# Optimization experiments

Hardware: AMD Instinct MI355X
Metric: run time of the kernel (lower is better)

Reference implementation:

```python
import jax, jax.numpy as jnp
import numpy as np

N_HEADS = 16
D_MODEL = 1024
D_K = D_MODEL // N_HEADS


def setup_inputs() -> dict:
    key = jax.random.key(0)
    ks = jax.random.split(key, 7)
    B, S = 2, 2048
    init = 0.02
    return {
        "query": jax.random.normal(ks[0], (B, S, D_MODEL), dtype=jnp.float32),
        "key": jax.random.normal(ks[1], (B, S, D_MODEL), dtype=jnp.float32),
        "value": jax.random.normal(ks[2], (B, S, D_MODEL), dtype=jnp.float32),
        "W_q": jax.random.normal(ks[3], (D_MODEL, D_MODEL), dtype=jnp.float32) * init,
        "W_k": jax.random.normal(ks[4], (D_MODEL, D_MODEL), dtype=jnp.float32) * init,
        "W_v": jax.random.normal(ks[5], (D_MODEL, D_MODEL), dtype=jnp.float32) * init,
        "W_o": jax.random.normal(ks[6], (D_MODEL, D_MODEL), dtype=jnp.float32) * init,
    }


def _split_heads(x):
    # (B, S, d_model) -> (B, H, S, d_k)
    B, S, _ = x.shape
    return x.reshape(B, S, N_HEADS, D_K).transpose(0, 2, 1, 3)


def reference(query, key, value, W_q, W_k, W_v, W_o):
    scale = jnp.sqrt(jnp.asarray(D_K, dtype=query.dtype))
    # torch Linear: y = x @ W.T
    Q = _split_heads(query @ W_q.T)   # (B,H,Sq,dk)
    K = _split_heads(key @ W_k.T)     # (B,H,Sk,dk)
    V = _split_heads(value @ W_v.T)   # (B,H,Sk,dk)
    scores = jnp.einsum("bhqd,bhkd->bhqk", Q, K) / scale
    attn = jax.nn.softmax(scores, axis=-1)           # (B,H,Sq,Sk); dropout p=0 -> identity
    attn_weights = attn.mean(axis=1)                 # (B,Sq,Sk) interpretable weights
    head_out = jnp.einsum("bhqk,bhkd->bqhd", attn, V)  # (B,Sq,H,dk)
    # NOTE: the original computes a head-gating (W_h) whose result is overwritten
    # by the concat below -> dead code, omitted.
    B, Sq = head_out.shape[0], head_out.shape[1]
    out = head_out.reshape(B, Sq, D_MODEL) @ W_o.T   # (B,Sq,d_model)
    return (out, attn_weights)
```

## Files before the change

kernel.cpp:

```cpp
#include <hip/hip_runtime.h>
#include <hip/hip_bf16.h>

#define Bq 2
#define Hh 16
#define Ss 2048
#define Dm 1024
#define Dk 64
#define QSC 0.18033688f

typedef _Float16 f16x8 __attribute__((ext_vector_type(8)));
typedef _Float16 f16x4 __attribute__((ext_vector_type(4)));
typedef _Float16 f16x2 __attribute__((ext_vector_type(2)));
typedef float    f32x4 __attribute__((ext_vector_type(4)));


__device__ __forceinline__ void gl_lds16(const void* g, void* lds) {
    __builtin_amdgcn_global_load_lds(
        (const __attribute__((address_space(1))) void*)g,
        (__attribute__((address_space(3))) void*)lds, 16, 0, 0);
}

extern "C" __device__ float __ocml_exp2_f32(float);

__device__ __forceinline__ float exp2_fast(float x) {
#if __has_builtin(__builtin_amdgcn_exp2f)
    return __builtin_amdgcn_exp2f(x);
#else
    return __ocml_exp2_f32(x);
#endif
}

__device__ __forceinline__ float rcp_fast(float x) {
#if __has_builtin(__builtin_amdgcn_rcpf)
    return __builtin_amdgcn_rcpf(x);
#else
    float r; asm("v_rcp_f32 %0, %1" : "=v"(r) : "v"(x)); return r;
#endif
}

__device__ __forceinline__ f16x2 pk_f16(float a, float b) {
    return __builtin_bit_cast(f16x2, __builtin_amdgcn_cvt_pkrtz(a, b));
}

__global__ __launch_bounds__(256) void convert_kernel(
    const float* __restrict__ q, const float* __restrict__ k,
    const float* __restrict__ v, const float* __restrict__ wq,
    const float* __restrict__ wk, const float* __restrict__ wv,
    const float* __restrict__ wo,
    _Float16* __restrict__ qd, _Float16* __restrict__ kd,
    _Float16* __restrict__ vd, _Float16* __restrict__ wd)
{
    int seg = blockIdx.y;
    const float* src; _Float16* dst; int n4;
    switch (seg) {
        case 0: src = q; dst = qd; n4 = 1048576; break;
        case 1: src = k; dst = kd; n4 = 1048576; break;
        case 2: src = v; dst = vd; n4 = 1048576; break;
        default:
            src = (seg == 3) ? wq : (seg == 4) ? wk : (seg == 5) ? wv : wo;
            dst = wd + (size_t)(seg - 3) * 1048576;
            n4 = 262144;
    }
    for (int i = blockIdx.x * 256 + threadIdx.x; i < n4; i += gridDim.x * 256) {
        float4 x = ((const float4*)src)[i];
        f16x4 h = {(_Float16)x.x, (_Float16)x.y, (_Float16)x.z, (_Float16)x.w};
        ((f16x4*)dst)[i] = h;
    }
}

__global__ __launch_bounds__(256) void gemm_qkv(
    const _Float16* __restrict__ qf, const _Float16* __restrict__ kf,
    const _Float16* __restrict__ vf, const _Float16* __restrict__ Wh,
    _Float16* __restrict__ Qd, _Float16* __restrict__ Kd,
    _Float16* __restrict__ Vd)
{
    __shared__ _Float16 As[128 * 32];
    __shared__ _Float16 Ws[128 * 32];
    int z = blockIdx.z;
    const _Float16* A = (z == 0) ? qf : (z == 1) ? kf : vf;
    const _Float16* W = Wh + (size_t)z * (Dm * Dm);
    int t = threadIdx.x, lane = t & 63, w = t >> 6;
    int quad = lane >> 4, l15 = lane & 15;
    int wm = w & 1, wn = w >> 1;
    int n0 = blockIdx.x * 128, m0 = blockIdx.y * 128;

    f32x4 acc[4][4] = {};
    for (int k0 = 0; k0 < Dm; k0 += 32) {
        __syncthreads();
        for (int j = 0; j < 2; ++j) {
            int ca = w * 128 + j * 64 + lane;
            int row = ca >> 2, c8 = (ca & 3) * 8;
            gl_lds16(&A[(size_t)(m0 + row) * Dm + k0 + c8],
                     &As[(size_t)(w * 128 + j * 64) * 8]);
            gl_lds16(&W[(size_t)(n0 + row) * Dm + k0 + c8],
                     &Ws[(size_t)(w * 128 + j * 64) * 8]);
        }
        __syncthreads();
        f16x8 af[4], bf[4];
        for (int mi = 0; mi < 4; ++mi)
            af[mi] = *(const f16x8*)&As[(wm * 64 + mi * 16 + l15) * 32 + quad * 8];
        for (int ni = 0; ni < 4; ++ni)
            bf[ni] = *(const f16x8*)&Ws[(wn * 64 + ni * 16 + l15) * 32 + quad * 8];
        for (int mi = 0; mi < 4; ++mi)
            for (int ni = 0; ni < 4; ++ni)
                acc[mi][ni] = __builtin_amdgcn_mfma_f32_16x16x32_f16(
                    af[mi], bf[ni], acc[mi][ni], 0, 0, 0);
    }
    _Float16* Y = (z == 0) ? Qd : (z == 1) ? Kd : Vd;
    float osc = (z == 0) ? QSC : 1.0f;
    for (int mi = 0; mi < 4; ++mi)
        for (int ni = 0; ni < 4; ++ni)
            for (int r = 0; r < 4; ++r) {
                int m = m0 + wm * 64 + mi * 16 + quad * 4 + r;
                int n = n0 + wn * 64 + ni * 16 + l15;
                int b = m >> 11, s = m & (Ss - 1);
                int h = n >> 6,  d = n & 63;
                _Float16 v = (_Float16)(acc[mi][ni][r] * osc);
                if (z < 2)
                    Y[(((size_t)(b * Hh + h) * Ss + s) << 6) + d] = v;
                else
                    Y[((size_t)(b * Hh + h) * Dk + d) * Ss + s] = v;
            }
}

__global__ __launch_bounds__(256) void gemm_out(
    const _Float16* __restrict__ HO, const _Float16* __restrict__ Woh,
    float* __restrict__ out)
{
    __shared__ _Float16 As[128 * 32];
    __shared__ _Float16 Ws[64 * 32];
    int t = threadIdx.x, lane = t & 63, w = t >> 6;
    int quad = lane >> 4, l15 = lane & 15;
    int n0 = blockIdx.x * 64, m0 = blockIdx.y * 128;

    f32x4 acc[2][4] = {};
    for (int k0 = 0; k0 < Dm; k0 += 32) {
        __syncthreads();
        for (int j = 0; j < 2; ++j) {
            int ca = w * 128 + j * 64 + lane;
            int row = ca >> 2, c8 = (ca & 3) * 8;
            gl_lds16(&HO[(size_t)(m0 + row) * Dm + k0 + c8],
                     &As[(size_t)(w * 128 + j * 64) * 8]);
        }
        {
            int cw = w * 64 + lane;
            int row = cw >> 2, c8 = (cw & 3) * 8;
            gl_lds16(&Woh[(size_t)(n0 + row) * Dm + k0 + c8],
                     &Ws[(size_t)(w * 64) * 8]);
        }
        __syncthreads();
        f16x8 af[2], bf[4];
        for (int mi = 0; mi < 2; ++mi)
            af[mi] = *(const f16x8*)&As[(w * 32 + mi * 16 + l15) * 32 + quad * 8];
        for (int ni = 0; ni < 4; ++ni)
            bf[ni] = *(const f16x8*)&Ws[(ni * 16 + l15) * 32 + quad * 8];
        for (int mi = 0; mi < 2; ++mi)
            for (int ni = 0; ni < 4; ++ni)
                acc[mi][ni] = __builtin_amdgcn_mfma_f32_16x16x32_f16(
                    af[mi], bf[ni], acc[mi][ni], 0, 0, 0);
    }
    for (int mi = 0; mi < 2; ++mi)
        for (int ni = 0; ni < 4; ++ni)
            for (int r = 0; r < 4; ++r) {
                int m = m0 + w * 32 + mi * 16 + quad * 4 + r;
                int n = n0 + ni * 16 + l15;
                out[(size_t)m * Dm + n] = acc[mi][ni][r];
            }
}

__global__ __launch_bounds__(256) void flash_kernel(
    const _Float16* __restrict__ Qh, const _Float16* __restrict__ Kh,
    const _Float16* __restrict__ Vt, _Float16* __restrict__ Op,
    float* __restrict__ lp)
{
    __shared__ alignas(16) _Float16 Ks[64][72];
    __shared__ alignas(16) _Float16 Vs[64][72];
    __shared__ alignas(16) _Float16 Ps[4][32][72];
    int t = threadIdx.x;
    int lane = t & 63, w = t >> 6;
    int quad = lane >> 4, l15 = lane & 15;
    int bh = blockIdx.x;
    int q0 = blockIdx.y * 128 + w * 32;
    int ks = blockIdx.z;
    int kt0 = ks * 16, kt1 = kt0 + 16;

    const _Float16* Qp = Qh + (size_t)bh * Ss * Dk;
    const _Float16* Kp = Kh + (size_t)bh * Ss * Dk;
    const _Float16* Vp = Vt + (size_t)bh * Dk * Ss;

    f16x8 qf[2][2];
    for (int qh = 0; qh < 2; ++qh)
        for (int kf = 0; kf < 2; ++kf)
            qf[qh][kf] = *(const f16x8*)
                &Qp[(size_t)(q0 + qh * 16 + l15) * Dk + kf * 32 + quad * 8];

    const _Float16 one = (_Float16)1.0f;
    const f16x8 ones = {one, one, one, one, one, one, one, one};

    int row0 = t >> 3,         col0 = (t & 7) * 8;
    int row1 = (256 + t) >> 3, col1 = col0;

    f16x8 kr0 = *(const f16x8*)&Kp[(size_t)(kt0 * 64 + row0) * Dk + col0];
    f16x8 kr1 = *(const f16x8*)&Kp[(size_t)(kt0 * 64 + row1) * Dk + col1];
    f16x8 vr0 = *(const f16x8*)&Vp[(size_t)row0 * Ss + kt0 * 64 + col0];
    f16x8 vr1 = *(const f16x8*)&Vp[(size_t)row1 * Ss + kt0 * 64 + col1];

    f32x4 o_acc[2][4] = {};
    f32x4 l_acc[2] = {};

    for (int kt = kt0; kt < kt1; ++kt) {
        __syncthreads();
        *(f16x8*)&Ks[row0][col0] = kr0;
        *(f16x8*)&Ks[row1][col1] = kr1;
        *(f16x8*)&Vs[row0][col0] = vr0;
        *(f16x8*)&Vs[row1][col1] = vr1;
        if (kt + 1 < kt1) {
            kr0 = *(const f16x8*)&Kp[(size_t)((kt + 1) * 64 + row0) * Dk + col0];
            kr1 = *(const f16x8*)&Kp[(size_t)((kt + 1) * 64 + row1) * Dk + col1];
            vr0 = *(const f16x8*)&Vp[(size_t)row0 * Ss + (kt + 1) * 64 + col0];
            vr1 = *(const f16x8*)&Vp[(size_t)row1 * Ss + (kt + 1) * 64 + col1];
        }
        __syncthreads();

        for (int nt = 0; nt < 4; ++nt) {
            f16x8 kf0 = *(const f16x8*)&Ks[nt * 16 + l15][quad * 8];
            f16x8 kf1 = *(const f16x8*)&Ks[nt * 16 + l15][32 + quad * 8];
            for (int qh = 0; qh < 2; ++qh) {
                f32x4 z = {};
                z = __builtin_amdgcn_mfma_f32_16x16x32_f16(kf0, qf[qh][0], z, 0, 0, 0);
                z = __builtin_amdgcn_mfma_f32_16x16x32_f16(kf1, qf[qh][1], z, 0, 0, 0);
                f16x2 h0 = pk_f16(exp2_fast(z[0]), exp2_fast(z[1]));
                f16x2 h1 = pk_f16(exp2_fast(z[2]), exp2_fast(z[3]));
                f16x4 hv = {h0[0], h0[1], h1[0], h1[1]};
                *(f16x4*)&Ps[w][qh * 16 + l15][nt * 16 + quad * 4] = hv;
            }
        }

        f16x8 vf[4][2];
        for (int dt = 0; dt < 4; ++dt) {
            vf[dt][0] = *(const f16x8*)&Vs[dt * 16 + l15][quad * 8];
            vf[dt][1] = *(const f16x8*)&Vs[dt * 16 + l15][32 + quad * 8];
        }
        for (int qh = 0; qh < 2; ++qh) {
            f16x8 pf0 = *(const f16x8*)&Ps[w][qh * 16 + l15][quad * 8];
            f16x8 pf1 = *(const f16x8*)&Ps[w][qh * 16 + l15][32 + quad * 8];
            l_acc[qh] = __builtin_amdgcn_mfma_f32_16x16x32_f16(
                pf0, ones, l_acc[qh], 0, 0, 0);
            l_acc[qh] = __builtin_amdgcn_mfma_f32_16x16x32_f16(
                pf1, ones, l_acc[qh], 0, 0, 0);
            for (int dt = 0; dt < 4; ++dt) {
                o_acc[qh][dt] = __builtin_amdgcn_mfma_f32_16x16x32_f16(
                    pf0, vf[dt][0], o_acc[qh][dt], 0, 0, 0);
                o_acc[qh][dt] = __builtin_amdgcn_mfma_f32_16x16x32_f16(
                    pf1, vf[dt][1], o_acc[qh][dt], 0, 0, 0);
            }
        }
    }

    _Float16* Od = Op + (size_t)ks * (Bq * Hh * Ss * Dk) + (size_t)bh * Ss * Dk;
    for (int qh = 0; qh < 2; ++qh) {
        for (int dt = 0; dt < 4; ++dt)
            for (int r = 0; r < 4; ++r) {
                int q = q0 + qh * 16 + quad * 4 + r;
                Od[(size_t)q * Dk + dt * 16 + l15] = (_Float16)o_acc[qh][dt][r];
            }
        if (l15 == 0)
            for (int r = 0; r < 4; ++r)
                lp[(size_t)ks * 65536 + (size_t)bh * Ss + q0 + qh * 16 +
                   quad * 4 + r] = l_acc[qh][r];
    }
}

__global__ __launch_bounds__(256) void reduce_kernel(
    const _Float16* __restrict__ Op, const float* __restrict__ lp,
    _Float16* __restrict__ HO, float* __restrict__ lw)
{
    int i = blockIdx.x * 256 + threadIdx.x;
    int d4  = i & 15;
    int row = i >> 4;
    f16x4 a = ((const f16x4*)Op)[i];
    f16x4 b = ((const f16x4*)Op)[i + 1048576];
    float l = lp[row] + lp[65536 + row];
    float inv = rcp_fast(l);
    int bh = row >> 11, q = row & (Ss - 1);
    int b_ = bh >> 4,  h = bh & 15;
    f16x4 o;
    for (int j = 0; j < 4; ++j)
        o[j] = (_Float16)(((float)a[j] + (float)b[j]) * inv);
    *(f16x4*)&HO[((size_t)(b_ * Ss + q)) * Dm + h * Dk + d4 * 4] = o;
    if (d4 == 0) lw[row] = l;
}

__global__ __launch_bounds__(256) void attn_mean_kernel(
    const _Float16* __restrict__ Qh, const _Float16* __restrict__ Kh,
    const float* __restrict__ lw, float* __restrict__ out_attn)
{
    __shared__ alignas(16) _Float16 Ks[64][72];
    int t = threadIdx.x;
    int lane = t & 63, w = t >> 6;
    int quad = lane >> 4, l15 = lane & 15;
    int k0 = blockIdx.x * 64;
    int q0 = blockIdx.y * 128;
    int b  = blockIdx.z;
    int qrow = q0 + w * 32;

    int srow0 = t >> 3, scol0 = (t & 7) * 8;
    int srow1 = (256 + t) >> 3, scol1 = scol0;

    f16x8 kr0, kr1, qn[2][2];
    float4 ln[2];
    {
        size_t base = (size_t)(b * Hh) * Ss;
        kr0 = *(const f16x8*)&Kh[(base + k0 + srow0) * Dk + scol0];
        kr1 = *(const f16x8*)&Kh[(base + k0 + srow1) * Dk + scol1];
        for (int qh = 0; qh < 2; ++qh) {
            qn[qh][0] = *(const f16x8*)&Qh[(base + qrow + qh * 16 + l15) * Dk + quad * 8];
            qn[qh][1] = *(const f16x8*)&Qh[(base + qrow + qh * 16 + l15) * Dk + 32 + quad * 8];
            ln[qh] = *(const float4*)&lw[base + qrow + qh * 16 + quad * 4];
        }
    }

    f32x4 acc[2][4] = {};
    for (int h = 0; h < Hh; ++h) {
        __syncthreads();
        *(f16x8*)&Ks[srow0][scol0] = kr0;
        *(f16x8*)&Ks[srow1][scol1] = kr1;
        f16x8 qf[2][2];
        float4 lv[2];
        for (int qh = 0; qh < 2; ++qh) {
            qf[qh][0] = qn[qh][0]; qf[qh][1] = qn[qh][1]; lv[qh] = ln[qh];
        }
        if (h < Hh - 1) {
            size_t base = (size_t)(b * Hh + h + 1) * Ss;
            kr0 = *(const f16x8*)&Kh[(base + k0 + srow0) * Dk + scol0];
            kr1 = *(const f16x8*)&Kh[(base + k0 + srow1) * Dk + scol1];
            for (int qh = 0; qh < 2; ++qh) {
                qn[qh][0] = *(const f16x8*)&Qh[(base + qrow + qh * 16 + l15) * Dk + quad * 8];
                qn[qh][1] = *(const f16x8*)&Qh[(base + qrow + qh * 16 + l15) * Dk + 32 + quad * 8];
                ln[qh] = *(const float4*)&lw[base + qrow + qh * 16 + quad * 4];
            }
        }
        __syncthreads();

        float ir[2][4];
        for (int qh = 0; qh < 2; ++qh) {
            ir[qh][0] = rcp_fast(lv[qh].x); ir[qh][1] = rcp_fast(lv[qh].y);
            ir[qh][2] = rcp_fast(lv[qh].z); ir[qh][3] = rcp_fast(lv[qh].w);
        }
        for (int nt = 0; nt < 4; ++nt) {
            f16x8 b0 = *(const f16x8*)&Ks[nt * 16 + l15][quad * 8];
            f16x8 b1 = *(const f16x8*)&Ks[nt * 16 + l15][32 + quad * 8];
            for (int qh = 0; qh < 2; ++qh) {
                f32x4 z = {};
                z = __builtin_amdgcn_mfma_f32_16x16x32_f16(qf[qh][0], b0, z, 0, 0, 0);
                z = __builtin_amdgcn_mfma_f32_16x16x32_f16(qf[qh][1], b1, z, 0, 0, 0);
                for (int r = 0; r < 4; ++r)
                    acc[qh][nt][r] += exp2_fast(z[r]) * ir[qh][r];
            }
        }
    }

    for (int qh = 0; qh < 2; ++qh)
        for (int nt = 0; nt < 4; ++nt)
            for (int r = 0; r < 4; ++r) {
                int q = qrow + qh * 16 + quad * 4 + r;
                out_attn[((size_t)(b * Ss + q)) * Ss + k0 + nt * 16 + l15] =
                    acc[qh][nt][r] * (1.0f / Hh);
            }
}

extern "C" void kernel_launch(void* const* d_in, const int* in_sizes, int n_in,
                              void* d_out, int out_size, void* d_ws, size_t ws_size,
                              hipStream_t stream) {
    const float* query = (const float*)d_in[0];
    const float* key   = (const float*)d_in[1];
    const float* value = (const float*)d_in[2];
    const float* Wq    = (const float*)d_in[3];
    const float* Wk    = (const float*)d_in[4];
    const float* Wv    = (const float*)d_in[5];
    const float* Wo    = (const float*)d_in[6];

    float* out      = (float*)d_out;
    float* attn_out = out + (size_t)4194304;

    _Float16* HO  = (_Float16*)attn_out;
    _Float16* qf  = (_Float16*)(attn_out + 2097152);
    _Float16* kf  = qf + 4194304;
    _Float16* vf  = kf + 4194304;
    _Float16* Op  = qf;
    float*    lp  = (float*)(Op + 2 * 4194304);

    _Float16* Qh = (_Float16*)d_ws;
    _Float16* Kh = Qh + (size_t)4194304;
    _Float16* Vt = Kh + (size_t)4194304;
    _Float16* Wh = Vt + (size_t)4194304;
    float*    lw = (float*)(Wh + (size_t)4194304);

    convert_kernel<<<dim3(256, 7), 256, 0, stream>>>(
        query, key, value, Wq, Wk, Wv, Wo, qf, kf, vf, Wh);

    gemm_qkv<<<dim3(8, 32, 3), 256, 0, stream>>>(qf, kf, vf, Wh, Qh, Kh, Vt);

    flash_kernel<<<dim3(Bq * Hh, Ss / 128, 2), 256, 0, stream>>>(Qh, Kh, Vt, Op, lp);

    reduce_kernel<<<4096, 256, 0, stream>>>(Op, lp, HO, lw);

    gemm_out<<<dim3(16, 32), 256, 0, stream>>>(HO, Wh + (size_t)3 * 1048576, out);

    attn_mean_kernel<<<dim3(Ss / 64, Ss / 128, Bq), 256, 0, stream>>>(
        Qh, Kh, lw, attn_out);
}
```

Measured before the change: 273.9 us.

## Double-buffer K/V via async LDS loads, keep P in registers

The flash and head-averaged attention kernels now stage K and V tiles with global_load_lds into double-buffered, XOR-swizzled LDS, so the next tile's load overlaps compute and one barrier per iteration is removed. In the flash kernel the softmax probabilities no longer go through an LDS buffer: they are rearranged into MFMA operand layout with cross-lane shuffles. The row sum is now built from scalar adds plus a final xor-shuffle reduction, replacing the extra MFMA against a ones vector. The trade-offs are many more shuffle instructions and reliance on the barrier waiting for the async loads to finish.

```diff
diff --git a/kernel.cpp b/kernel.cpp
--- a/kernel.cpp
+++ b/kernel.cpp
@@ -12,6 +12,7 @@
 typedef _Float16 f16x4 __attribute__((ext_vector_type(4)));
 typedef _Float16 f16x2 __attribute__((ext_vector_type(2)));
 typedef float    f32x4 __attribute__((ext_vector_type(4)));
+typedef unsigned int u32x4 __attribute__((ext_vector_type(4)));
 
 
 __device__ __forceinline__ void gl_lds16(const void* g, void* lds) {
@@ -38,8 +39,8 @@
 #endif
 }
 
-__device__ __forceinline__ f16x2 pk_f16(float a, float b) {
-    return __builtin_bit_cast(f16x2, __builtin_amdgcn_cvt_pkrtz(a, b));
+__device__ __forceinline__ unsigned int pk_u32(float a, float b) {
+    return __builtin_bit_cast(unsigned int, __builtin_amdgcn_cvt_pkrtz(a, b));
 }
 
 __global__ __launch_bounds__(256) void convert_kernel(
@@ -173,9 +174,7 @@
     const _Float16* __restrict__ Vt, _Float16* __restrict__ Op,
     float* __restrict__ lp)
 {
-    __shared__ alignas(16) _Float16 Ks[64][72];
-    __shared__ alignas(16) _Float16 Vs[64][72];
-    __shared__ alignas(16) _Float16 Ps[4][32][72];
+    __shared__ alignas(16) _Float16 KV[2][2][4096];
     int t = threadIdx.x;
     int lane = t & 63, w = t >> 6;
     int quad = lane >> 4, l15 = lane & 15;
@@ -185,89 +184,139 @@
     int kt0 = ks * 16, kt1 = kt0 + 16;
 
     const _Float16* Qp = Qh + (size_t)bh * Ss * Dk;
-    const _Float16* Kp = Kh + (size_t)bh * Ss * Dk;
-    const _Float16* Vp = Vt + (size_t)bh * Dk * Ss;
+    const char* Kp = (const char*)(Kh + (size_t)bh * Ss * Dk);
+    const char* Vp = (const char*)(Vt + (size_t)bh * Dk * Ss);
 
     f16x8 qf[2][2];
+#pragma unroll
     for (int qh = 0; qh < 2; ++qh)
+#pragma unroll
         for (int kf = 0; kf < 2; ++kf)
             qf[qh][kf] = *(const f16x8*)
                 &Qp[(size_t)(q0 + qh * 16 + l15) * Dk + kf * 32 + quad * 8];
 
-    const _Float16 one = (_Float16)1.0f;
-    const f16x8 ones = {one, one, one, one, one, one, one, one};
-
-    int row0 = t >> 3,         col0 = (t & 7) * 8;
-    int row1 = (256 + t) >> 3, col1 = col0;
-
-    f16x8 kr0 = *(const f16x8*)&Kp[(size_t)(kt0 * 64 + row0) * Dk + col0];
-    f16x8 kr1 = *(const f16x8*)&Kp[(size_t)(kt0 * 64 + row1) * Dk + col1];
-    f16x8 vr0 = *(const f16x8*)&Vp[(size_t)row0 * Ss + kt0 * 64 + col0];
-    f16x8 vr1 = *(const f16x8*)&Vp[(size_t)row1 * Ss + kt0 * 64 + col1];
+    int srow = t >> 3;
+    int scolb = (t & 7) * 16;
+    int iA = (((2 * quad) & 3) << 4) | l15;
+    int iB = ((((2 * quad) + 1) & 3) << 4) | l15;
+    bool lo = (quad < 2);
+    int swz = (l15 & 7) << 4;
+
+#define FSTAGE(kt, buf)                                                        \
+    {                                                                          \
+        const char* Kt = Kp + (size_t)(kt) * 8192;                             \
+        const char* Vb = Vp + (kt) * 128;                                      \
+        char* KD = (char*)&KV[buf][0][0];                                      \
+        char* VD = (char*)&KV[buf][1][0];                                      \
+        _Pragma("unroll")                                                      \
+        for (int hf = 0; hf < 2; ++hf) {                                       \
+            int r = srow + hf * 32;                                            \
+            int sc = scolb ^ ((r & 7) << 4);                                   \
+            gl_lds16(Kt + r * 128 + sc, KD + r * 128 + scolb);                 \
+            gl_lds16(Vb + (size_t)r * 4096 + sc, VD + r * 128 + scolb);        \
+        }                                                                      \
+    }
 
     f32x4 o_acc[2][4] = {};
-    f32x4 l_acc[2] = {};
-
+    float lsum[2] = {0.f, 0.f};
+
+    FSTAGE(kt0, 0);
     for (int kt = kt0; kt < kt1; ++kt) {
-        __syncthreads();
-        *(f16x8*)&Ks[row0][col0] = kr0;
-        *(f16x8*)&Ks[row1][col1] = kr1;
-        *(f16x8*)&Vs[row0][col0] = vr0;
-        *(f16x8*)&Vs[row1][col1] = vr1;
-        if (kt + 1 < kt1) {
-            kr0 = *(const f16x8*)&Kp[(size_t)((kt + 1) * 64 + row0) * Dk + col0];
-            kr1 = *(const f16x8*)&Kp[(size_t)((kt + 1) * 64 + row1) * Dk + col1];
-            vr0 = *(const f16x8*)&Vp[(size_t)row0 * Ss + (kt + 1) * 64 + col0];
-            vr1 = *(const f16x8*)&Vp[(size_t)row1 * Ss + (kt + 1) * 64 + col1];
-        }
-        __syncthreads();
-
+        int buf = (kt - kt0) & 1;
+        __syncthreads();
+        if (kt + 1 < kt1) FSTAGE(kt + 1, buf ^ 1);
+        const char* Ksb = (const char*)&KV[buf][0][0];
+        const char* Vsb = (const char*)&KV[buf][1][0];
+
+        unsigned int cu[2][4][2];
+#pragma unroll
         for (int nt = 0; nt < 4; ++nt) {
-            f16x8 kf0 = *(const f16x8*)&Ks[nt * 16 + l15][quad * 8];
-            f16x8 kf1 = *(const f16x8*)&Ks[nt * 16 + l15][32 + quad * 8];
+            int rb = (nt * 16 + l15) << 7;
+            f16x8 kf0 = *(const f16x8*)(Ksb + rb + ((quad * 16) ^ swz));
+            f16x8 kf1 = *(const f16x8*)(Ksb + rb + ((64 + quad * 16) ^ swz));
+#pragma unroll
             for (int qh = 0; qh < 2; ++qh) {
                 f32x4 z = {};
                 z = __builtin_amdgcn_mfma_f32_16x16x32_f16(kf0, qf[qh][0], z, 0, 0, 0);
                 z = __builtin_amdgcn_mfma_f32_16x16x32_f16(kf1, qf[qh][1], z, 0, 0, 0);
-                f16x2 h0 = pk_f16(exp2_fast(z[0]), exp2_fast(z[1]));
-                f16x2 h1 = pk_f16(exp2_fast(z[2]), exp2_fast(z[3]));
-                f16x4 hv = {h0[0], h0[1], h1[0], h1[1]};
-                *(f16x4*)&Ps[w][qh * 16 + l15][nt * 16 + quad * 4] = hv;
-            }
-        }
-
-        f16x8 vf[4][2];
+                float e0 = exp2_fast(z[0]), e1 = exp2_fast(z[1]);
+                float e2 = exp2_fast(z[2]), e3 = exp2_fast(z[3]);
+                lsum[qh] += (e0 + e1) + (e2 + e3);
+                cu[qh][nt][0] = pk_u32(e0, e1);
+                cu[qh][nt][1] = pk_u32(e2, e3);
+            }
+        }
+
+        f16x8 pf[2][2];
+#pragma unroll
+        for (int qh = 0; qh < 2; ++qh) {
+            unsigned int d0, d1, d2, d3, d4, d5, d6, d7;
+            {
+                unsigned int xa, xb;
+                xa = (unsigned)__shfl((int)cu[qh][0][0], iA);
+                xb = (unsigned)__shfl((int)cu[qh][1][0], iA);
+                d0 = lo ? xa : xb;
+                xa = (unsigned)__shfl((int)cu[qh][0][1], iA);
+                xb = (unsigned)__shfl((int)cu[qh][1][1], iA);
+                d1 = lo ? xa : xb;
+                xa = (unsigned)__shfl((int)cu[qh][0][0], iB);
+                xb = (unsigned)__shfl((int)cu[qh][1][0], iB);
+                d2 = lo ? xa : xb;
+                xa = (unsigned)__shfl((int)cu[qh][0][1], iB);
+                xb = (unsigned)__shfl((int)cu[qh][1][1], iB);
+                d3 = lo ? xa : xb;
+                xa = (unsigned)__shfl((int)cu[qh][2][0], iA);
+                xb = (unsigned)__shfl((int)cu[qh][3][0], iA);
+                d4 = lo ? xa : xb;
+                xa = (unsigned)__shfl((int)cu[qh][2][1], iA);
+                xb = (unsigned)__shfl((int)cu[qh][3][1], iA);
+                d5 = lo ? xa : xb;
+                xa = (unsigned)__shfl((int)cu[qh][2][0], iB);
+                xb = (unsigned)__shfl((int)cu[qh][3][0], iB);
+                d6 = lo ? xa : xb;
+                xa = (unsigned)__shfl((int)cu[qh][2][1], iB);
+                xb = (unsigned)__shfl((int)cu[qh][3][1], iB);
+                d7 = lo ? xa : xb;
+            }
+            u32x4 p0 = {d0, d1, d2, d3};
+            u32x4 p1 = {d4, d5, d6, d7};
+            pf[qh][0] = __builtin_bit_cast(f16x8, p0);
+            pf[qh][1] = __builtin_bit_cast(f16x8, p1);
+        }
+#pragma unroll
         for (int dt = 0; dt < 4; ++dt) {
-            vf[dt][0] = *(const f16x8*)&Vs[dt * 16 + l15][quad * 8];
-            vf[dt][1] = *(const f16x8*)&Vs[dt * 16 + l15][32 + quad * 8];
-        }
-        for (int qh = 0; qh < 2; ++qh) {
-            f16x8 pf0 = *(const f16x8*)&Ps[w][qh * 16 + l15][quad * 8];
-            f16x8 pf1 = *(const f16x8*)&Ps[w][qh * 16 + l15][32 + quad * 8];
-            l_acc[qh] = __builtin_amdgcn_mfma_f32_16x16x32_f16(
-                pf0, ones, l_acc[qh], 0, 0, 0);
-            l_acc[qh] = __builtin_amdgcn_mfma_f32_16x16x32_f16(
-                pf1, ones, l_acc[qh], 0, 0, 0);
-            for (int dt = 0; dt < 4; ++dt) {
+            int rb = (dt * 16 + l15) << 7;
+            f16x8 vf0 = *(const f16x8*)(Vsb + rb + ((quad * 16) ^ swz));
+            f16x8 vf1 = *(const f16x8*)(Vsb + rb + ((64 + quad * 16) ^ swz));
+#pragma unroll
+            for (int qh = 0; qh < 2; ++qh) {
                 o_acc[qh][dt] = __builtin_amdgcn_mfma_f32_16x16x32_f16(
-                    pf0, vf[dt][0], o_acc[qh][dt], 0, 0, 0);
+                    pf[qh][0], vf0, o_acc[qh][dt], 0, 0, 0);
                 o_acc[qh][dt] = __builtin_amdgcn_mfma_f32_16x16x32_f16(
-                    pf1, vf[dt][1], o_acc[qh][dt], 0, 0, 0);
-            }
-        }
+                    pf[qh][1], vf1, o_acc[qh][dt], 0, 0, 0);
+            }
+        }
+    }
+#undef FSTAGE
+
+#pragma unroll
+    for (int qh = 0; qh < 2; ++qh) {
+        lsum[qh] += __shfl_xor(lsum[qh], 16);
+        lsum[qh] += __shfl_xor(lsum[qh], 32);
     }
 
     _Float16* Od = Op + (size_t)ks * (Bq * Hh * Ss * Dk) + (size_t)bh * Ss * Dk;
+#pragma unroll
     for (int qh = 0; qh < 2; ++qh) {
+#pragma unroll
         for (int dt = 0; dt < 4; ++dt)
+#pragma unroll
             for (int r = 0; r < 4; ++r) {
                 int q = q0 + qh * 16 + quad * 4 + r;
                 Od[(size_t)q * Dk + dt * 16 + l15] = (_Float16)o_acc[qh][dt][r];
             }
-        if (l15 == 0)
-            for (int r = 0; r < 4; ++r)
-                lp[(size_t)ks * 65536 + (size_t)bh * Ss + q0 + qh * 16 +
-                   quad * 4 + r] = l_acc[qh][r];
+        if (lane < 16)
+            lp[(size_t)ks * 65536 + (size_t)bh * Ss + q0 + qh * 16 + lane] = lsum[qh];
     }
 }
 
@@ -295,7 +344,7 @@
     const _Float16* __restrict__ Qh, const _Float16* __restrict__ Kh,
     const float* __restrict__ lw, float* __restrict__ out_attn)
 {
-    __shared__ alignas(16) _Float16 Ks[64][72];
+    __shared__ alignas(16) _Float16 KB[2][4096];
     int t = threadIdx.x;
     int lane = t & 63, w = t >> 6;
     int quad = lane >> 4, l15 = lane & 15;
@@ -303,65 +352,87 @@
     int q0 = blockIdx.y * 128;
     int b  = blockIdx.z;
     int qrow = q0 + w * 32;
-
-    int srow0 = t >> 3, scol0 = (t & 7) * 8;
-    int srow1 = (256 + t) >> 3, scol1 = scol0;
-
-    f16x8 kr0, kr1, qn[2][2];
+    int srow = t >> 3, scolb = (t & 7) * 16;
+    int swz = (l15 & 7) << 4;
+
+#define ASTAGE(h, buf)                                                         \
+    {                                                                          \
+        const char* Kt = (const char*)Kh +                                     \
+            ((size_t)(b * Hh + (h)) * Ss + k0) * 128;                          \
+        char* D = (char*)&KB[buf][0];                                          \
+        _Pragma("unroll")                                                      \
+        for (int hf = 0; hf < 2; ++hf) {                                       \
+            int r = srow + hf * 32;                                            \
+            int sc = scolb ^ ((r & 7) << 4);                                   \
+            gl_lds16(Kt + r * 128 + sc, D + r * 128 + scolb);                  \
+        }                                                                      \
+    }
+
+    f16x8 qn[2][2];
     float4 ln[2];
     {
         size_t base = (size_t)(b * Hh) * Ss;
-        kr0 = *(const f16x8*)&Kh[(base + k0 + srow0) * Dk + scol0];
-        kr1 = *(const f16x8*)&Kh[(base + k0 + srow1) * Dk + scol1];
+#pragma unroll
         for (int qh = 0; qh < 2; ++qh) {
             qn[qh][0] = *(const f16x8*)&Qh[(base + qrow + qh * 16 + l15) * Dk + quad * 8];
             qn[qh][1] = *(const f16x8*)&Qh[(base + qrow + qh * 16 + l15) * Dk + 32 + quad * 8];
             ln[qh] = *(const float4*)&lw[base + qrow + qh * 16 + quad * 4];
         }
     }
+    ASTAGE(0, 0);
 
     f32x4 acc[2][4] = {};
     for (int h = 0; h < Hh; ++h) {
-        __syncthreads();
-        *(f16x8*)&Ks[srow0][scol0] = kr0;
-        *(f16x8*)&Ks[srow1][scol1] = kr1;
+        int buf = h & 1;
+        __syncthreads();
+        if (h + 1 < Hh) ASTAGE(h + 1, buf ^ 1);
+
         f16x8 qf[2][2];
         float4 lv[2];
+#pragma unroll
         for (int qh = 0; qh < 2; ++qh) {
             qf[qh][0] = qn[qh][0]; qf[qh][1] = qn[qh][1]; lv[qh] = ln[qh];
         }
         if (h < Hh - 1) {
             size_t base = (size_t)(b * Hh + h + 1) * Ss;
-            kr0 = *(const f16x8*)&Kh[(base + k0 + srow0) * Dk + scol0];
-            kr1 = *(const f16x8*)&Kh[(base + k0 + srow1) * Dk + scol1];
+#pragma unroll
             for (int qh = 0; qh < 2; ++qh) {
                 qn[qh][0] = *(const f16x8*)&Qh[(base + qrow + qh * 16 + l15) * Dk + quad * 8];
                 qn[qh][1] = *(const f16x8*)&Qh[(base + qrow + qh * 16 + l15) * Dk + 32 + quad * 8];
                 ln[qh] = *(const float4*)&lw[base + qrow + qh * 16 + quad * 4];
             }
         }
-        __syncthreads();
 
         float ir[2][4];
+#pragma unroll
         for (int qh = 0; qh < 2; ++qh) {
             ir[qh][0] = rcp_fast(lv[qh].x); ir[qh][1] = rcp_fast(lv[qh].y);
             ir[qh][2] = rcp_fast(lv[qh].z); ir[qh][3] = rcp_fast(lv[qh].w);
         }
+        const char* Ksb = (const char*)&KB[buf][0];
+#pragma unroll
         for (int nt = 0; nt < 4; ++nt) {
-            f16x8 b0 = *(const f16x8*)&Ks[nt * 16 + l15][quad * 8];
-            f16x8 b1 = *(const f16x8*)&Ks[nt * 16 + l15][32 + quad * 8];
+            int rb = (nt * 16 + l15) << 7;
+            f16x8 b0 = *(const f16x8*)(Ksb + rb + ((quad * 16) ^ swz));
+            f16x8 b1 = *(const f16x8*)(Ksb + rb + ((64 + quad * 16) ^ swz));
+#pragma unroll
             for (int qh = 0; qh < 2; ++qh) {
                 f32x4 z = {};
                 z = __builtin_amdgcn_mfma_f32_16x16x32_f16(qf[qh][0], b0, z, 0, 0, 0);
                 z = __builtin_amdgcn_mfma_f32_16x16x32_f16(qf[qh][1], b1, z, 0, 0, 0);
+#pragma unroll
                 for (int r = 0; r < 4; ++r)
                     acc[qh][nt][r] += exp2_fast(z[r]) * ir[qh][r];
             }
         }
     }
-
+#undef ASTAGE
+
+#pragma unroll
     for (int qh = 0; qh < 2; ++qh)
+#pragma unroll
         for (int nt = 0; nt < 4; ++nt)
+#pragma unroll
             for (int r = 0; r < 4; ++r) {
                 int q = qrow + qh * 16 + quad * 4 + r;
                 out_attn[((size_t)(b * Ss + q)) * Ss + k0 + nt * 16 + l15] =
```

Result: slower. 300.4 us (+9.7%).
